# Optimization experiments

Measured on AMD Instinct MI355X. Metric: run time of the kernel, lower is better.

Reference implementation:

```python
import jax, jax.numpy as jnp
import numpy as np

N_NODES = 50000
N_EDGES = 800000
IN_CH = 128
HID = 64
HEADS = 4
OUT_CH = 10
N_GRAPHS = 512
NEG_SLOPE = 0.2


def setup_inputs() -> dict:
    key = jax.random.key(0)
    ks = jax.random.split(key, 16)
    x = jax.random.normal(ks[0], (N_NODES, IN_CH), dtype=jnp.float32)
    edge_index = jax.random.randint(ks[1], (2, N_EDGES), 0, N_NODES, dtype=jnp.int64)
    batch = jnp.sort(jax.random.randint(ks[2], (N_NODES,), 0, N_GRAPHS, dtype=jnp.int64))
    s = 1.0 / np.sqrt(IN_CH)
    W1 = jax.random.uniform(ks[3], (IN_CH, HEADS * HID), jnp.float32, -s, s)
    att_src1 = jax.random.normal(ks[4], (HEADS, HID), jnp.float32) * 0.1
    att_dst1 = jax.random.normal(ks[5], (HEADS, HID), jnp.float32) * 0.1
    b1 = jnp.zeros((HEADS * HID,), jnp.float32)
    s2 = 1.0 / np.sqrt(HEADS * HID)
    W2 = jax.random.uniform(ks[6], (HEADS * HID, HID), jnp.float32, -s2, s2)
    att_src2 = jax.random.normal(ks[7], (1, HID), jnp.float32) * 0.1
    att_dst2 = jax.random.normal(ks[8], (1, HID), jnp.float32) * 0.1
    b2 = jnp.zeros((HID,), jnp.float32)
    s3 = 1.0 / np.sqrt(HID)
    Wl = jax.random.uniform(ks[9], (HID, OUT_CH), jnp.float32, -s3, s3)
    bl = jnp.zeros((OUT_CH,), jnp.float32)
    return dict(x=x, edge_index=edge_index, batch=batch,
                W1=W1, att_src1=att_src1, att_dst1=att_dst1, b1=b1,
                W2=W2, att_src2=att_src2, att_dst2=att_dst2, b2=b2,
                Wl=Wl, bl=bl)


def gat_conv(x, src, dst, W, att_src, att_dst, bias, heads, out_ch, concat):
    """PyG GATConv: gather -> per-edge attention -> segment softmax over dst -> scatter-add."""
    n = x.shape[0]
    h = (x @ W).reshape(n, heads, out_ch)            # [N,H,C]
    a_s = jnp.sum(h * att_src, axis=-1)              # [N,H]
    a_d = jnp.sum(h * att_dst, axis=-1)              # [N,H]
    e = jax.nn.leaky_relu(a_s[src] + a_d[dst], NEG_SLOPE)  # [E,H]
    m = jax.ops.segment_max(e, dst, num_segments=n)  # stable softmax per dst
    alpha = jnp.exp(e - m[dst])
    denom = jax.ops.segment_sum(alpha, dst, num_segments=n)
    alpha = alpha / denom[dst]
    out = jax.ops.segment_sum(h[src] * alpha[:, :, None], dst, num_segments=n)  # [N,H,C]
    if concat:
        out = out.reshape(n, heads * out_ch)
    else:
        out = out.mean(axis=1)
    return out + bias


def reference(x, edge_index, batch, W1, att_src1, att_dst1, b1,
              W2, att_src2, att_dst2, b2, Wl, bl):
    n = x.shape[0]
    # PyG GATConv default add_self_loops=True
    loops = jnp.arange(n, dtype=edge_index.dtype)
    src = jnp.concatenate([edge_index[0], loops])
    dst = jnp.concatenate([edge_index[1], loops])

    h = jax.nn.elu(gat_conv(x, src, dst, W1, att_src1, att_dst1, b1, HEADS, HID, True))
    h = jax.nn.elu(gat_conv(h, src, dst, W2, att_src2, att_dst2, b2, 1, HID, False))

    # global_mean_pool
    sums = jax.ops.segment_sum(h, batch, num_segments=N_GRAPHS)
    cnts = jax.ops.segment_sum(jnp.ones((n,), h.dtype), batch, num_segments=N_GRAPHS)
    pooled = sums / jnp.maximum(cnts, 1.0)[:, None]

    return pooled @ Wl + bl
```

## Files before the change

### kernel.cpp

```cpp
#include <hip/hip_runtime.h>
#include <hip/hip_bf16.h>
#include <math.h>

#define N_NODES 50000
#define N_EDGES 800000
#define IN_CH 128
#define HID 64
#define HEADS 4
#define OUT_CH 10
#define N_GRAPHS 512
#define NEG_SLOPE 0.2f

#define ETOT_C (N_EDGES + N_NODES)
#define NPB 128
#define NBUK ((N_NODES + NPB - 1) / NPB)
#define EPB 2048
#define GA ((ETOT_C + EPB - 1) / EPB)
#define GB1 ((N_NODES + 63) / 64)
#define GZ 32
#define GW 192

using short8_t = __attribute__((ext_vector_type(8))) short;
using f32x4 = __attribute__((ext_vector_type(4))) float;

__device__ __forceinline__ float b2f(unsigned short u) {
    return __uint_as_float(((unsigned)u) << 16);
}
__device__ __forceinline__ unsigned short f2b(float f) {
    __hip_bfloat16 b = __float2bfloat16(f);
    return *(unsigned short*)&b;
}
__device__ __forceinline__ short f2bs(float f) {
    __hip_bfloat16 b = __float2bfloat16(f);
    return *(short*)&b;
}
__device__ __forceinline__ float lrelu(float x) { return x > 0.f ? x : NEG_SLOPE * x; }

__global__ __launch_bounds__(256) void megaA_k(
        const int* __restrict__ dst, unsigned* __restrict__ bcnt,
        const int* __restrict__ batch, float* __restrict__ cntf,
        float* __restrict__ pooled,
        const float* __restrict__ W1, const float* __restrict__ W2,
        unsigned short* __restrict__ Wt1, unsigned short* __restrict__ Wt2) {
    int b = blockIdx.x;
    int t = threadIdx.x;
    if (b < GA) {
        __shared__ unsigned bins[NBUK];
        for (int i = t; i < NBUK; i += 256) bins[i] = 0;
        __syncthreads();
        int e0 = b * EPB;
        int e1 = min(e0 + EPB, ETOT_C);
        for (int i = e0 + t; i < e1; i += 256) {
            int d = (i < N_EDGES) ? dst[i] : i - N_EDGES;
            atomicAdd(&bins[d >> 7], 1u);
        }
        __syncthreads();
        for (int i = t; i < NBUK; i += 256)
            if (bins[i]) atomicAdd(&bcnt[i], bins[i]);
        return;
    }
    b -= GA;
    if (b < 2) {
        int g = b * 256 + t;
        if (g >= N_GRAPHS) return;
        int lo = 0, hi = N_NODES;
        while (lo < hi) { int mid = (lo + hi) >> 1; if (batch[mid] < g) lo = mid + 1; else hi = mid; }
        int lo2 = lo, hi2 = N_NODES;
        while (lo2 < hi2) { int mid = (lo2 + hi2) >> 1; if (batch[mid] < g + 1) lo2 = mid + 1; else hi2 = mid; }
        cntf[g] = (float)(lo2 - lo);
        return;
    }
    b -= 2;
    if (b < GZ) {
        int idx = b * 256 + t;
        *(float4*)&pooled[(size_t)idx * 4] = make_float4(0.f, 0.f, 0.f, 0.f);
        return;
    }
    b -= GZ;
    int idx = b * 256 + t;
    if (idx < 256 * 128) {
        int n = idx / 128, k = idx % 128;
        Wt1[idx] = f2b(W1[(size_t)k * 256 + n]);
    }
    int j = idx - 256 * 128;
    if (j >= 0 && j < 64 * 256) {
        int n = j / 256, k = j % 256;
        Wt2[j] = f2b(W2[(size_t)k * 64 + n]);
    }
}

__global__ void scanB_k(const unsigned* __restrict__ bcnt, int* __restrict__ bbase,
                        unsigned* __restrict__ bcur) {
    __shared__ int tmp[512];
    int t = threadIdx.x;
    int v = (t < NBUK) ? (int)bcnt[t] : 0;
    tmp[t] = v;
    __syncthreads();
    for (int o = 1; o < 512; o <<= 1) {
        int u = (t >= o) ? tmp[t - o] : 0;
        __syncthreads();
        tmp[t] += u;
        __syncthreads();
    }
    if (t < NBUK) {
        int ex = tmp[t] - v;
        bbase[t] = ex;
        bcur[t] = (unsigned)ex;
    }
    if (t == NBUK - 1) bbase[NBUK] = tmp[t];
}

__global__ __launch_bounds__(256) void megaB_k(
        const float* __restrict__ X, const unsigned short* __restrict__ Wt,
        unsigned short* __restrict__ Yb,
        const float* __restrict__ asrc, const float* __restrict__ adst,
        float* __restrict__ As, float* __restrict__ Ad, int M,
        const int* __restrict__ src, const int* __restrict__ dst,
        unsigned* __restrict__ bcur, int2* __restrict__ ebuf) {
    int b = blockIdx.x;
    if (b < GB1) {
        const int lane = threadIdx.x & 63;
        const int w = threadIdx.x >> 6;
        const int r0 = b * 64 + w * 16;
        const int l15 = lane & 15;
        const int rc = min(r0 + l15, M - 1);
        const int kg = (lane >> 4) * 8;

        f32x4 acc[16] = {};
#pragma unroll
        for (int kc = 0; kc < 4; kc++) {
            int k0 = kc * 32 + kg;
            float4 xa = *(const float4*)&X[(size_t)rc * 128 + k0];
            float4 xb = *(const float4*)&X[(size_t)rc * 128 + k0 + 4];
            short8_t af;
            af[0] = f2bs(xa.x); af[1] = f2bs(xa.y); af[2] = f2bs(xa.z); af[3] = f2bs(xa.w);
            af[4] = f2bs(xb.x); af[5] = f2bs(xb.y); af[6] = f2bs(xb.z); af[7] = f2bs(xb.w);
#pragma unroll
            for (int ct = 0; ct < 16; ct++) {
                int col = ct * 16 + l15;
                short8_t bf = *(const short8_t*)&Wt[(size_t)col * 128 + k0];
                acc[ct] = __builtin_amdgcn_mfma_f32_16x16x32_bf16(af, bf, acc[ct], 0, 0, 0);
            }
        }

        const int rbase = r0 + (lane >> 4) * 4;
#pragma unroll
        for (int reg = 0; reg < 4; reg++) {
            int gr = rbase + reg;
            float s0 = 0.f, s1 = 0.f, s2 = 0.f, s3 = 0.f;
            float d0 = 0.f, d1 = 0.f, d2 = 0.f, d3 = 0.f;
#pragma unroll
            for (int cg = 0; cg < 4; cg++) {
                int c = cg * 16 + l15;
                float v0 = acc[0 * 4 + cg][reg], v1 = acc[1 * 4 + cg][reg];
                float v2 = acc[2 * 4 + cg][reg], v3 = acc[3 * 4 + cg][reg];
                s0 += v0 * asrc[0 * 64 + c]; d0 += v0 * adst[0 * 64 + c];
                s1 += v1 * asrc[1 * 64 + c]; d1 += v1 * adst[1 * 64 + c];
                s2 += v2 * asrc[2 * 64 + c]; d2 += v2 * adst[2 * 64 + c];
                s3 += v3 * asrc[3 * 64 + c]; d3 += v3 * adst[3 * 64 + c];
            }
#pragma unroll
            for (int o = 8; o > 0; o >>= 1) {
                s0 += __shfl_xor(s0, o); d0 += __shfl_xor(d0, o);
                s1 += __shfl_xor(s1, o); d1 += __shfl_xor(d1, o);
                s2 += __shfl_xor(s2, o); d2 += __shfl_xor(d2, o);
                s3 += __shfl_xor(s3, o); d3 += __shfl_xor(d3, o);
            }
            if (l15 == 0 && gr < M) {
                *(float4*)&As[gr * 4] = make_float4(s0, s1, s2, s3);
                *(float4*)&Ad[gr * 4] = make_float4(d0, d1, d2, d3);
            }
        }
#pragma unroll
        for (int reg = 0; reg < 4; reg++) {
            int gr = rbase + reg;
            if (gr >= M) continue;
#pragma unroll
            for (int cg = 0; cg < 4; cg++) {
                int c = cg * 16 + l15;
                ushort4 p;
                p.x = f2b(acc[0 * 4 + cg][reg]);
                p.y = f2b(acc[1 * 4 + cg][reg]);
                p.z = f2b(acc[2 * 4 + cg][reg]);
                p.w = f2b(acc[3 * 4 + cg][reg]);
                *(ushort4*)&Yb[(size_t)gr * 256 + c * 4] = p;
            }
        }
        return;
    }
    b -= GB1;
    {
        __shared__ unsigned bins[NBUK];
        __shared__ unsigned bbl[NBUK];
        __shared__ int dstash[EPB];
        int t = threadIdx.x;
        for (int i = t; i < NBUK; i += 256) bins[i] = 0;
        __syncthreads();
        int e0 = b * EPB;
        int e1 = min(e0 + EPB, ETOT_C);
        for (int i = e0 + t; i < e1; i += 256) {
            int d = (i < N_EDGES) ? dst[i] : i - N_EDGES;
            dstash[i - e0] = d;
            atomicAdd(&bins[d >> 7], 1u);
        }
        __syncthreads();
        for (int i = t; i < NBUK; i += 256) {
            bbl[i] = bins[i] ? atomicAdd(&bcur[i], bins[i]) : 0u;
        }
        __syncthreads();
        for (int i = t; i < NBUK; i += 256) bins[i] = 0;
        __syncthreads();
        for (int i = e0 + t; i < e1; i += 256) {
            int d = dstash[i - e0];
            int s = (i < N_EDGES) ? src[i] : i - N_EDGES;
            unsigned r = atomicAdd(&bins[d >> 7], 1u);
            ebuf[bbl[d >> 7] + r] = make_int2(s, d);
        }
    }
}

__global__ __launch_bounds__(256) void passC_k(const int* __restrict__ bbase,
                                               const int2* __restrict__ ebuf,
                                               int* __restrict__ rowptr,
                                               int* __restrict__ csrc) {
    __shared__ int cnt[NPB];
    __shared__ int loc[NPB];
    __shared__ int cur[NPB];
    int b = blockIdx.x;
    int t = threadIdx.x;
    int base = bbase[b], end = bbase[b + 1];
    if (t < NPB) cnt[t] = 0;
    __syncthreads();
    for (int j = base + t; j < end; j += 256) {
        int2 e = ebuf[j];
        atomicAdd(&cnt[e.y & (NPB - 1)], 1);
    }
    __syncthreads();
    if (t < NPB) loc[t] = cnt[t];
    __syncthreads();
    for (int o = 1; o < NPB; o <<= 1) {
        int v = (t < NPB && t >= o) ? loc[t - o] : 0;
        __syncthreads();
        if (t < NPB) loc[t] += v;
        __syncthreads();
    }
    if (t < NPB) {
        int node = b * NPB + t;
        if (node < N_NODES) rowptr[node] = base + loc[t] - cnt[t];
        cur[t] = 0;
    }
    if (b == NBUK - 1 && t == 0) rowptr[N_NODES] = end;
    __syncthreads();
    for (int j = base + t; j < end; j += 256) {
        int2 e = ebuf[j];
        int n = e.y & (NPB - 1);
        int r = atomicAdd(&cur[n], 1);
        csrc[base + loc[n] - cnt[n] + r] = e.x;
    }
}

__global__ __launch_bounds__(256) void mfma_gemm2_k(
        const unsigned short* __restrict__ Xb, const unsigned short* __restrict__ Wt,
        unsigned short* __restrict__ Yb,
        const float* __restrict__ asrc, const float* __restrict__ adst,
        float* __restrict__ As, float* __restrict__ Ad, int M) {
    const int lane = threadIdx.x & 63;
    const int w = threadIdx.x >> 6;
    const int r0 = blockIdx.x * 64 + w * 16;
    const int l15 = lane & 15;
    const int rc = min(r0 + l15, M - 1);
    const int kg = (lane >> 4) * 8;

    f32x4 acc[4] = {};
#pragma unroll
    for (int kc = 0; kc < 8; kc++) {
        int k0 = kc * 32 + kg;
        short8_t af = *(const short8_t*)&Xb[(size_t)rc * 256 + k0];
#pragma unroll
        for (int ct = 0; ct < 4; ct++) {
            int col = ct * 16 + l15;
            short8_t bf = *(const short8_t*)&Wt[(size_t)col * 256 + k0];
            acc[ct] = __builtin_amdgcn_mfma_f32_16x16x32_bf16(af, bf, acc[ct], 0, 0, 0);
        }
    }

    const int rbase = r0 + (lane >> 4) * 4;
#pragma unroll
    for (int reg = 0; reg < 4; reg++) {
        int gr = rbase + reg;
        float sv = 0.f, dv = 0.f;
#pragma unroll
        for (int ct = 0; ct < 4; ct++) {
            int c = ct * 16 + l15;
            float v = acc[ct][reg];
            sv += v * asrc[c];
            dv += v * adst[c];
        }
#pragma unroll
        for (int o = 8; o > 0; o >>= 1) { sv += __shfl_xor(sv, o); dv += __shfl_xor(dv, o); }
        if (l15 == 0 && gr < M) { As[gr] = sv; Ad[gr] = dv; }
        if (gr < M) {
#pragma unroll
            for (int ct = 0; ct < 4; ct++)
                Yb[(size_t)gr * 64 + ct * 16 + l15] = f2b(acc[ct][reg]);
        }
    }
}

__global__ void agg1_k(const int* __restrict__ rowptr, const int* __restrict__ csrc,
                       const float* __restrict__ As, const float* __restrict__ Ad,
                       const __hip_bfloat16* __restrict__ Hb,
                       const float* __restrict__ bias,
                       unsigned short* __restrict__ Outb, int nnodes) {
    __shared__ int ssh[4][64];
    __shared__ float4 wsh[4][64];
    int lane = threadIdx.x & 63;
    int w = threadIdx.x >> 6;
    int node = blockIdx.x * 4 + w;
    int beg = rowptr[node], end = rowptr[node + 1];
    int deg = end - beg;
    const unsigned short* hb = (const unsigned short*)Hb;
    float4 bv = *(const float4*)&Ad[node * 4];
    bool fast = (deg <= 64);
    if (fast) {
        bool act = lane < deg;
        int s = act ? csrc[beg + lane] : 0;
        float4 a = *(const float4*)&As[s * 4];
        float e0 = lrelu(a.x + bv.x), e1 = lrelu(a.y + bv.y);
        float e2 = lrelu(a.z + bv.z), e3 = lrelu(a.w + bv.w);
        if (!act) { e0 = e1 = e2 = e3 = -INFINITY; }
        float m0 = e0, m1 = e1, m2 = e2, m3 = e3;
#pragma unroll
        for (int o = 32; o > 0; o >>= 1) {
            m0 = fmaxf(m0, __shfl_xor(m0, o)); m1 = fmaxf(m1, __shfl_xor(m1, o));
            m2 = fmaxf(m2, __shfl_xor(m2, o)); m3 = fmaxf(m3, __shfl_xor(m3, o));
        }
        float x0 = act ? __expf(e0 - m0) : 0.f;
        float x1 = act ? __expf(e1 - m1) : 0.f;
        float x2 = act ? __expf(e2 - m2) : 0.f;
        float x3 = act ? __expf(e3 - m3) : 0.f;
        float d0 = x0, d1 = x1, d2 = x2, d3 = x3;
#pragma unroll
        for (int o = 32; o > 0; o >>= 1) {
            d0 += __shfl_xor(d0, o); d1 += __shfl_xor(d1, o);
            d2 += __shfl_xor(d2, o); d3 += __shfl_xor(d3, o);
        }
        ssh[w][lane] = s;
        wsh[w][lane] = make_float4(x0 / d0, x1 / d1, x2 / d2, x3 / d3);
    }
    __syncthreads();
    float acc0 = 0.f, acc1 = 0.f, acc2 = 0.f, acc3 = 0.f;
    if (fast) {
        float p0 = 0.f, p1 = 0.f, p2 = 0.f, p3 = 0.f;
        int j = 0;
        for (; j + 4 <= deg; j += 4) {
            int sA = ssh[w][j], sB = ssh[w][j + 1], sC = ssh[w][j + 2], sD = ssh[w][j + 3];
            float4 wA = wsh[w][j], wB = wsh[w][j + 1], wC = wsh[w][j + 2], wD = wsh[w][j + 3];
            ushort4 vA = *(const ushort4*)&hb[(size_t)sA * 256 + lane * 4];
            ushort4 vB = *(const ushort4*)&hb[(size_t)sB * 256 + lane * 4];
            ushort4 vC = *(const ushort4*)&hb[(size_t)sC * 256 + lane * 4];
            ushort4 vD = *(const ushort4*)&hb[(size_t)sD * 256 + lane * 4];
            acc0 += wA.x * b2f(vA.x) + wC.x * b2f(vC.x);
            p0   += wB.x * b2f(vB.x) + wD.x * b2f(vD.x);
            acc1 += wA.y * b2f(vA.y) + wC.y * b2f(vC.y);
            p1   += wB.y * b2f(vB.y) + wD.y * b2f(vD.y);
            acc2 += wA.z * b2f(vA.z) + wC.z * b2f(vC.z);
            p2   += wB.z * b2f(vB.z) + wD.z * b2f(vD.z);
            acc3 += wA.w * b2f(vA.w) + wC.w * b2f(vC.w);
            p3   += wB.w * b2f(vB.w) + wD.w * b2f(vD.w);
        }
        for (; j < deg; j++) {
            int s = ssh[w][j];
            float4 wt = wsh[w][j];
            ushort4 v = *(const ushort4*)&hb[(size_t)s * 256 + lane * 4];
            acc0 += wt.x * b2f(v.x); acc1 += wt.y * b2f(v.y);
            acc2 += wt.z * b2f(v.z); acc3 += wt.w * b2f(v.w);
        }
        acc0 += p0; acc1 += p1; acc2 += p2; acc3 += p3;
    } else {
        float m0 = -INFINITY, m1 = -INFINITY, m2 = -INFINITY, m3 = -INFINITY;
        for (int j = beg + lane; j < end; j += 64) {
            float4 a = *(const float4*)&As[csrc[j] * 4];
            m0 = fmaxf(m0, lrelu(a.x + bv.x)); m1 = fmaxf(m1, lrelu(a.y + bv.y));
            m2 = fmaxf(m2, lrelu(a.z + bv.z)); m3 = fmaxf(m3, lrelu(a.w + bv.w));
        }
#pragma unroll
        for (int o = 32; o > 0; o >>= 1) {
            m0 = fmaxf(m0, __shfl_xor(m0, o)); m1 = fmaxf(m1, __shfl_xor(m1, o));
            m2 = fmaxf(m2, __shfl_xor(m2, o)); m3 = fmaxf(m3, __shfl_xor(m3, o));
        }
        float d0 = 0.f, d1 = 0.f, d2 = 0.f, d3 = 0.f;
        for (int j = beg + lane; j < end; j += 64) {
            float4 a = *(const float4*)&As[csrc[j] * 4];
            d0 += __expf(lrelu(a.x + bv.x) - m0); d1 += __expf(lrelu(a.y + bv.y) - m1);
            d2 += __expf(lrelu(a.z + bv.z) - m2); d3 += __expf(lrelu(a.w + bv.w) - m3);
        }
#pragma unroll
        for (int o = 32; o > 0; o >>= 1) {
            d0 += __shfl_xor(d0, o); d1 += __shfl_xor(d1, o);
            d2 += __shfl_xor(d2, o); d3 += __shfl_xor(d3, o);
        }
        for (int j = beg; j < end; j++) {
            int s = csrc[j];
            float4 a = *(const float4*)&As[s * 4];
            float w0 = __expf(lrelu(a.x + bv.x) - m0) / d0;
            float w1 = __expf(lrelu(a.y + bv.y) - m1) / d1;
            float w2 = __expf(lrelu(a.z + bv.z) - m2) / d2;
            float w3 = __expf(lrelu(a.w + bv.w) - m3) / d3;
            ushort4 v = *(const ushort4*)&hb[(size_t)s * 256 + lane * 4];
            acc0 += w0 * b2f(v.x); acc1 += w1 * b2f(v.y);
            acc2 += w2 * b2f(v.z); acc3 += w3 * b2f(v.w);
        }
    }
    float r0 = acc0 + bias[0 * 64 + lane];
    float r1 = acc1 + bias[1 * 64 + lane];
    float r2 = acc2 + bias[2 * 64 + lane];
    float r3 = acc3 + bias[3 * 64 + lane];
    r0 = r0 > 0.f ? r0 : expm1f(r0);
    r1 = r1 > 0.f ? r1 : expm1f(r1);
    r2 = r2 > 0.f ? r2 : expm1f(r2);
    r3 = r3 > 0.f ? r3 : expm1f(r3);
    size_t base = (size_t)node * 256;
    Outb[base + 0 * 64 + lane] = f2b(r0);
    Outb[base + 1 * 64 + lane] = f2b(r1);
    Outb[base + 2 * 64 + lane] = f2b(r2);
    Outb[base + 3 * 64 + lane] = f2b(r3);
}

__global__ void agg2_k(const int* __restrict__ rowptr, const int* __restrict__ csrc,
                       const float* __restrict__ As, const float* __restrict__ Ad,
                       const __hip_bfloat16* __restrict__ Hb,
                       const float* __restrict__ bias, const int* __restrict__ batch,
                       float* __restrict__ pooled, int nnodes) {
    __shared__ int ssh[4][64];
    __shared__ float wsh[4][64];
    int lane = threadIdx.x & 63;
    int w = threadIdx.x >> 6;
    int node = blockIdx.x * 4 + w;
    int beg = rowptr[node], end = rowptr[node + 1];
    int deg = end - beg;
    const unsigned short* hb = (const unsigned short*)Hb;
    float ad = Ad[node];
    bool fast = (deg <= 64);
    if (fast) {
        bool act = lane < deg;
        int s = act ? csrc[beg + lane] : 0;
        float e = lrelu(As[s] + ad);
        if (!act) e = -INFINITY;
        float m = e;
#pragma unroll
        for (int o = 32; o > 0; o >>= 1) m = fmaxf(m, __shfl_xor(m, o));
        float x = act ? __expf(e - m) : 0.f;
        float d = x;
#pragma unroll
        for (int o = 32; o > 0; o >>= 1) d += __shfl_xor(d, o);
        ssh[w][lane] = s;
        wsh[w][lane] = x / d;
    }
    __syncthreads();
    float acc = 0.f;
    if (fast) {
        float p = 0.f;
        int j = 0;
        for (; j + 4 <= deg; j += 4) {
            int sA = ssh[w][j], sB = ssh[w][j + 1], sC = ssh[w][j + 2], sD = ssh[w][j + 3];
            float wA = wsh[w][j], wB = wsh[w][j + 1], wC = wsh[w][j + 2], wD = wsh[w][j + 3];
            acc += wA * b2f(hb[(size_t)sA * 64 + lane]) + wC * b2f(hb[(size_t)sC * 64 + lane]);
            p   += wB * b2f(hb[(size_t)sB * 64 + lane]) + wD * b2f(hb[(size_t)sD * 64 + lane]);
        }
        for (; j < deg; j++) acc += wsh[w][j] * b2f(hb[(size_t)ssh[w][j] * 64 + lane]);
        acc += p;
    } else {
        float m = -INFINITY;
        for (int j = beg + lane; j < end; j += 64) m = fmaxf(m, lrelu(As[csrc[j]] + ad));
#pragma unroll
        for (int o = 32; o > 0; o >>= 1) m = fmaxf(m, __shfl_xor(m, o));
        float d = 0.f;
        for (int j = beg + lane; j < end; j += 64) d += __expf(lrelu(As[csrc[j]] + ad) - m);
#pragma unroll
        for (int o = 32; o > 0; o >>= 1) d += __shfl_xor(d, o);
        for (int j = beg; j < end; j++) {
            int s = csrc[j];
            float wt = __expf(lrelu(As[s] + ad) - m) / d;
            acc += wt * b2f(hb[(size_t)s * 64 + lane]);
        }
    }
    float v = acc + bias[lane];
    v = v > 0.f ? v : expm1f(v);
    atomicAdd(&pooled[batch[node] * 64 + lane], v);
}

__global__ void final_k(const float* __restrict__ pooled, const float* __restrict__ cnt,
                        const float* __restrict__ Wl, const float* __restrict__ bl,
                        float* __restrict__ out) {
    int g = blockIdx.x;
    int t = threadIdx.x;
    __shared__ float s[64];
    float c = cnt[g];
    c = c > 1.f ? c : 1.f;
    s[t] = pooled[g * 64 + t] / c;
    __syncthreads();
    if (t < OUT_CH) {
        float acc = bl[t];
        for (int k = 0; k < 64; k++) acc += s[k] * Wl[k * OUT_CH + t];
        out[g * OUT_CH + t] = acc;
    }
}

extern "C" void kernel_launch(void* const* d_in, const int* in_sizes, int n_in,
                              void* d_out, int out_size, void* d_ws, size_t ws_size,
                              hipStream_t stream) {
    const float* x    = (const float*)d_in[0];
    const int*   ei   = (const int*)d_in[1];
    const int*   batch= (const int*)d_in[2];
    const float* W1   = (const float*)d_in[3];
    const float* as1  = (const float*)d_in[4];
    const float* ad1  = (const float*)d_in[5];
    const float* b1   = (const float*)d_in[6];
    const float* W2   = (const float*)d_in[7];
    const float* as2  = (const float*)d_in[8];
    const float* ad2  = (const float*)d_in[9];
    const float* b2   = (const float*)d_in[10];
    const float* Wl   = (const float*)d_in[11];
    const float* bl   = (const float*)d_in[12];
    float* out = (float*)d_out;

    const int* src = ei;
    const int* dst = ei + N_EDGES;

    char* ws = (char*)d_ws;
    size_t off = 0;
    auto alloc = [&](size_t bytes) {
        void* p = ws + off;
        off = (off + bytes + 255) & ~((size_t)255);
        return p;
    };
    unsigned short* h1b  = (unsigned short*)alloc((size_t)N_NODES * 256 * 2);
    unsigned short* out1b= (unsigned short*)alloc((size_t)N_NODES * 256 * 2);
    float* As1    = (float*)alloc((size_t)N_NODES * 4 * 4);
    float* Ad1    = (float*)alloc((size_t)N_NODES * 4 * 4);
    float* As2    = (float*)alloc((size_t)N_NODES * 4);
    float* Ad2    = (float*)alloc((size_t)N_NODES * 4);
    int*   rowptr = (int*)  alloc((size_t)(N_NODES + 1) * 4);
    int*   csrc   = (int*)  alloc((size_t)ETOT_C * 4);
    int2*  ebuf   = (int2*) alloc((size_t)ETOT_C * 8);
    unsigned* bcnt= (unsigned*)alloc((size_t)NBUK * 4);
    int*   bbase  = (int*)  alloc((size_t)(NBUK + 1) * 4);
    unsigned* bcur= (unsigned*)alloc((size_t)NBUK * 4);
    unsigned short* Wt1 = (unsigned short*)alloc((size_t)256 * 128 * 2);
    unsigned short* Wt2 = (unsigned short*)alloc((size_t)64 * 256 * 2);
    float* pooled = (float*)alloc((size_t)N_GRAPHS * 64 * 4);
    float* cntf   = (float*)alloc((size_t)N_GRAPHS * 4);
    unsigned short* h2b = h1b;

    hipMemsetAsync(bcnt, 0, (size_t)NBUK * 4, stream);

    megaA_k<<<GA + 2 + GZ + GW, 256, 0, stream>>>(dst, bcnt, batch, cntf, pooled,
                                                  W1, W2, Wt1, Wt2);
    scanB_k<<<1, 512, 0, stream>>>(bcnt, bbase, bcur);

    megaB_k<<<GB1 + GA, 256, 0, stream>>>(x, Wt1, h1b, as1, ad1, As1, Ad1, N_NODES,
                                          src, dst, bcur, ebuf);
    passC_k<<<NBUK, 256, 0, stream>>>(bbase, ebuf, rowptr, csrc);

    agg1_k<<<N_NODES / 4, 256, 0, stream>>>(rowptr, csrc, As1, Ad1,
                                            (const __hip_bfloat16*)h1b, b1, out1b, N_NODES);

    mfma_gemm2_k<<<(N_NODES + 63) / 64, 256, 0, stream>>>(out1b, Wt2, h2b, as2, ad2,
                                                          As2, Ad2, N_NODES);
    agg2_k<<<N_NODES / 4, 256, 0, stream>>>(rowptr, csrc, As2, Ad2,
                                            (const __hip_bfloat16*)h2b, b2, batch, pooled, N_NODES);

    final_k<<<N_GRAPHS, 64, 0, stream>>>(pooled, cntf, Wl, bl, out);
}
```

Before: 214.2 us.

## Split layer-1 aggregation into two head-pair passes with head-pair-major feature layout

```diff
diff --git a/kernel.cpp b/kernel.cpp
--- a/kernel.cpp
+++ b/kernel.cpp
@@ -19,6 +19,7 @@
 #define GB1 ((N_NODES + 63) / 64)
 #define GZ 32
 #define GW 192
+#define HPB (N_NODES / 4)
 
 using short8_t = __attribute__((ext_vector_type(8))) short;
 using f32x4 = __attribute__((ext_vector_type(4))) float;
@@ -178,12 +179,13 @@
 #pragma unroll
             for (int cg = 0; cg < 4; cg++) {
                 int c = cg * 16 + l15;
-                ushort4 p;
-                p.x = f2b(acc[0 * 4 + cg][reg]);
-                p.y = f2b(acc[1 * 4 + cg][reg]);
-                p.z = f2b(acc[2 * 4 + cg][reg]);
-                p.w = f2b(acc[3 * 4 + cg][reg]);
-                *(ushort4*)&Yb[(size_t)gr * 256 + c * 4] = p;
+                ushort2 p0, p1;
+                p0.x = f2b(acc[0 * 4 + cg][reg]);
+                p0.y = f2b(acc[1 * 4 + cg][reg]);
+                p1.x = f2b(acc[2 * 4 + cg][reg]);
+                p1.y = f2b(acc[3 * 4 + cg][reg]);
+                *(ushort2*)&Yb[(size_t)gr * 256 + c * 2] = p0;
+                *(ushort2*)&Yb[(size_t)gr * 256 + 128 + c * 2] = p1;
             }
         }
         return;
@@ -313,118 +315,98 @@
                        const float* __restrict__ bias,
                        unsigned short* __restrict__ Outb, int nnodes) {
     __shared__ int ssh[4][64];
-    __shared__ float4 wsh[4][64];
+    __shared__ float2 wsh[4][64];
     int lane = threadIdx.x & 63;
     int w = threadIdx.x >> 6;
-    int node = blockIdx.x * 4 + w;
+    int b = blockIdx.x;
+    int hp = b / HPB;
+    int node = (b % HPB) * 4 + w;
     int beg = rowptr[node], end = rowptr[node + 1];
     int deg = end - beg;
     const unsigned short* hb = (const unsigned short*)Hb;
-    float4 bv = *(const float4*)&Ad[node * 4];
+    float2 bv = *(const float2*)&Ad[node * 4 + hp * 2];
     bool fast = (deg <= 64);
     if (fast) {
         bool act = lane < deg;
         int s = act ? csrc[beg + lane] : 0;
-        float4 a = *(const float4*)&As[s * 4];
+        float2 a = *(const float2*)&As[s * 4 + hp * 2];
         float e0 = lrelu(a.x + bv.x), e1 = lrelu(a.y + bv.y);
-        float e2 = lrelu(a.z + bv.z), e3 = lrelu(a.w + bv.w);
-        if (!act) { e0 = e1 = e2 = e3 = -INFINITY; }
-        float m0 = e0, m1 = e1, m2 = e2, m3 = e3;
+        if (!act) { e0 = e1 = -INFINITY; }
+        float m0 = e0, m1 = e1;
 #pragma unroll
         for (int o = 32; o > 0; o >>= 1) {
             m0 = fmaxf(m0, __shfl_xor(m0, o)); m1 = fmaxf(m1, __shfl_xor(m1, o));
-            m2 = fmaxf(m2, __shfl_xor(m2, o)); m3 = fmaxf(m3, __shfl_xor(m3, o));
         }
         float x0 = act ? __expf(e0 - m0) : 0.f;
         float x1 = act ? __expf(e1 - m1) : 0.f;
-        float x2 = act ? __expf(e2 - m2) : 0.f;
-        float x3 = act ? __expf(e3 - m3) : 0.f;
-        float d0 = x0, d1 = x1, d2 = x2, d3 = x3;
+        float d0 = x0, d1 = x1;
 #pragma unroll
         for (int o = 32; o > 0; o >>= 1) {
             d0 += __shfl_xor(d0, o); d1 += __shfl_xor(d1, o);
-            d2 += __shfl_xor(d2, o); d3 += __shfl_xor(d3, o);
         }
         ssh[w][lane] = s;
-        wsh[w][lane] = make_float4(x0 / d0, x1 / d1, x2 / d2, x3 / d3);
-    }
-    __syncthreads();
-    float acc0 = 0.f, acc1 = 0.f, acc2 = 0.f, acc3 = 0.f;
+        wsh[w][lane] = make_float2(x0 / d0, x1 / d1);
+    }
+    __syncthreads();
+    float acc0 = 0.f, acc1 = 0.f;
     if (fast) {
-        float p0 = 0.f, p1 = 0.f, p2 = 0.f, p3 = 0.f;
+        float p0 = 0.f, p1 = 0.f;
         int j = 0;
         for (; j + 4 <= deg; j += 4) {
             int sA = ssh[w][j], sB = ssh[w][j + 1], sC = ssh[w][j + 2], sD = ssh[w][j + 3];
-            float4 wA = wsh[w][j], wB = wsh[w][j + 1], wC = wsh[w][j + 2], wD = wsh[w][j + 3];
-            ushort4 vA = *(const ushort4*)&hb[(size_t)sA * 256 + lane * 4];
-            ushort4 vB = *(const ushort4*)&hb[(size_t)sB * 256 + lane * 4];
-            ushort4 vC = *(const ushort4*)&hb[(size_t)sC * 256 + lane * 4];
-            ushort4 vD = *(const ushort4*)&hb[(size_t)sD * 256 + lane * 4];
+            float2 wA = wsh[w][j], wB = wsh[w][j + 1], wC = wsh[w][j + 2], wD = wsh[w][j + 3];
+            ushort2 vA = *(const ushort2*)&hb[(size_t)sA * 256 + hp * 128 + lane * 2];
+            ushort2 vB = *(const ushort2*)&hb[(size_t)sB * 256 + hp * 128 + lane * 2];
+            ushort2 vC = *(const ushort2*)&hb[(size_t)sC * 256 + hp * 128 + lane * 2];
+            ushort2 vD = *(const ushort2*)&hb[(size_t)sD * 256 + hp * 128 + lane * 2];
             acc0 += wA.x * b2f(vA.x) + wC.x * b2f(vC.x);
             p0   += wB.x * b2f(vB.x) + wD.x * b2f(vD.x);
             acc1 += wA.y * b2f(vA.y) + wC.y * b2f(vC.y);
             p1   += wB.y * b2f(vB.y) + wD.y * b2f(vD.y);
-            acc2 += wA.z * b2f(vA.z) + wC.z * b2f(vC.z);
-            p2   += wB.z * b2f(vB.z) + wD.z * b2f(vD.z);
-            acc3 += wA.w * b2f(vA.w) + wC.w * b2f(vC.w);
-            p3   += wB.w * b2f(vB.w) + wD.w * b2f(vD.w);
         }
         for (; j < deg; j++) {
             int s = ssh[w][j];
-            float4 wt = wsh[w][j];
-            ushort4 v = *(const ushort4*)&hb[(size_t)s * 256 + lane * 4];
+            float2 wt = wsh[w][j];
+            ushort2 v = *(const ushort2*)&hb[(size_t)s * 256 + hp * 128 + lane * 2];
             acc0 += wt.x * b2f(v.x); acc1 += wt.y * b2f(v.y);
-            acc2 += wt.z * b2f(v.z); acc3 += wt.w * b2f(v.w);
-        }
-        acc0 += p0; acc1 += p1; acc2 += p2; acc3 += p3;
+        }
+        acc0 += p0; acc1 += p1;
     } else {
-        float m0 = -INFINITY, m1 = -INFINITY, m2 = -INFINITY, m3 = -INFINITY;
+        float m0 = -INFINITY, m1 = -INFINITY;
         for (int j = beg + lane; j < end; j += 64) {
-            float4 a = *(const float4*)&As[csrc[j] * 4];
+            float2 a = *(const float2*)&As[csrc[j] * 4 + hp * 2];
             m0 = fmaxf(m0, lrelu(a.x + bv.x)); m1 = fmaxf(m1, lrelu(a.y + bv.y));
-            m2 = fmaxf(m2, lrelu(a.z + bv.z)); m3 = fmaxf(m3, lrelu(a.w + bv.w));
         }
 #pragma unroll
         for (int o = 32; o > 0; o >>= 1) {
             m0 = fmaxf(m0, __shfl_xor(m0, o)); m1 = fmaxf(m1, __shfl_xor(m1, o));
-            m2 = fmaxf(m2, __shfl_xor(m2, o)); m3 = fmaxf(m3, __shfl_xor(m3, o));
-        }
-        float d0 = 0.f, d1 = 0.f, d2 = 0.f, d3 = 0.f;
+        }
+        float d0 = 0.f, d1 = 0.f;
         for (int j = beg + lane; j < end; j += 64) {
-            float4 a = *(const float4*)&As[csrc[j] * 4];
+            float2 a = *(const float2*)&As[csrc[j] * 4 + hp * 2];
             d0 += __expf(lrelu(a.x + bv.x) - m0); d1 += __expf(lrelu(a.y + bv.y) - m1);
-            d2 += __expf(lrelu(a.z + bv.z) - m2); d3 += __expf(lrelu(a.w + bv.w) - m3);
         }
 #pragma unroll
         for (int o = 32; o > 0; o >>= 1) {
             d0 += __shfl_xor(d0, o); d1 += __shfl_xor(d1, o);
-            d2 += __shfl_xor(d2, o); d3 += __shfl_xor(d3, o);
         }
         for (int j = beg; j < end; j++) {
             int s = csrc[j];
-            float4 a = *(const float4*)&As[s * 4];
+            float2 a = *(const float2*)&As[s * 4 + hp * 2];
             float w0 = __expf(lrelu(a.x + bv.x) - m0) / d0;
             float w1 = __expf(lrelu(a.y + bv.y) - m1) / d1;
-            float w2 = __expf(lrelu(a.z + bv.z) - m2) / d2;
-            float w3 = __expf(lrelu(a.w + bv.w) - m3) / d3;
-            ushort4 v = *(const ushort4*)&hb[(size_t)s * 256 + lane * 4];
+            ushort2 v = *(const ushort2*)&hb[(size_t)s * 256 + hp * 128 + lane * 2];
             acc0 += w0 * b2f(v.x); acc1 += w1 * b2f(v.y);
-            acc2 += w2 * b2f(v.z); acc3 += w3 * b2f(v.w);
-        }
-    }
-    float r0 = acc0 + bias[0 * 64 + lane];
-    float r1 = acc1 + bias[1 * 64 + lane];
-    float r2 = acc2 + bias[2 * 64 + lane];
-    float r3 = acc3 + bias[3 * 64 + lane];
+        }
+    }
+    int h0 = hp * 2;
+    float r0 = acc0 + bias[h0 * 64 + lane];
+    float r1 = acc1 + bias[(h0 + 1) * 64 + lane];
     r0 = r0 > 0.f ? r0 : expm1f(r0);
     r1 = r1 > 0.f ? r1 : expm1f(r1);
-    r2 = r2 > 0.f ? r2 : expm1f(r2);
-    r3 = r3 > 0.f ? r3 : expm1f(r3);
     size_t base = (size_t)node * 256;
-    Outb[base + 0 * 64 + lane] = f2b(r0);
-    Outb[base + 1 * 64 + lane] = f2b(r1);
-    Outb[base + 2 * 64 + lane] = f2b(r2);
-    Outb[base + 3 * 64 + lane] = f2b(r3);
+    Outb[base + h0 * 64 + lane] = f2b(r0);
+    Outb[base + (h0 + 1) * 64 + lane] = f2b(r1);
 }
 
 __global__ void agg2_k(const int* __restrict__ rowptr, const int* __restrict__ csrc,
@@ -563,8 +545,8 @@
                                           src, dst, bcur, ebuf);
     passC_k<<<NBUK, 256, 0, stream>>>(bbase, ebuf, rowptr, csrc);
 
-    agg1_k<<<N_NODES / 4, 256, 0, stream>>>(rowptr, csrc, As1, Ad1,
-                                            (const __hip_bfloat16*)h1b, b1, out1b, N_NODES);
+    agg1_k<<<2 * HPB, 256, 0, stream>>>(rowptr, csrc, As1, Ad1,
+                                        (const __hip_bfloat16*)h1b, b1, out1b, N_NODES);
 
     mfma_gemm2_k<<<(N_NODES + 63) / 64, 256, 0, stream>>>(out1b, Wt2, h2b, as2, ad2,
                                                           As2, Ad2, N_NODES);
```

Measured after the change: 222.7 us. 3.9% more time.
